# Performance work log

Hardware: AMD Instinct MI355X
Metric: run time of the kernel (lower is better)

Reference implementation:

```python
import jax, jax.numpy as jnp
import numpy as np

BS, S, D, H, L, DEG = 16, 512, 256, 4, 6, 16
N = BS * S
E = N * DEG
DH = D // H
LN_EPS = 1e-5


def _ln(x, w, b):
    mu = jnp.mean(x, -1, keepdims=True)
    var = jnp.var(x, -1, keepdims=True)
    return (x - mu) * jax.lax.rsqrt(var + LN_EPS) * w + b


def _gine(x, src, dst, ea, eps, ew, eb, w1, b1, w2, b2):
    # PyG GINEConv: nn((1+eps)*x_i + sum_j relu(x_j + lin(e_ji))), msgs flow src->dst
    msg = jax.nn.relu(x[src] + ea @ ew.T + eb)
    agg = jax.ops.segment_sum(msg, dst, num_segments=x.shape[0])
    z = (1.0 + eps) * x + agg
    return jax.nn.relu(z @ w1.T + b1) @ w2.T + b2


def setup_inputs():
    key = jax.random.key(0)
    ks = iter(jax.random.split(key, 64))
    def rnd(shape, scale=0.05):
        return jax.random.normal(next(ks), shape, jnp.float32) * scale
    rng = np.random.default_rng(0)
    sl = rng.integers(0, S, E)
    dl = rng.integers(0, S, E)
    gid = np.repeat(np.arange(BS), S * DEG)
    edge_index = jnp.asarray(np.stack([sl + gid * S, dl + gid * S]), jnp.int32)
    ptr = jnp.asarray(np.arange(BS + 1) * S, jnp.int32)
    drop_edge_label = jnp.asarray(rng.integers(0, 2, E), jnp.int32)
    return dict(
        x=rnd((N, 2), 1.0),
        edge_attr=jax.random.uniform(next(ks), (E, 1), jnp.float32),
        eps1=jnp.zeros(()), edge_w1=rnd((2, 1)), edge_b1=jnp.zeros((2,)),
        nn1_w1=rnd((64, 2)), nn1_b1=jnp.zeros((64,)),
        nn1_w2=rnd((128, 64)), nn1_b2=jnp.zeros((128,)),
        eps2=jnp.zeros(()), edge_w2=rnd((128, 1)), edge_b2=jnp.zeros((128,)),
        nn2_w1=rnd((D, 128)), nn2_b1=jnp.zeros((D,)),
        nn2_w2=rnd((D, D)), nn2_b2=jnp.zeros((D,)),
        pos_emb=rnd((512, D), 0.02),
        in_proj_w=rnd((L, 3 * D, D)), in_proj_b=jnp.zeros((L, 3 * D)),
        out_proj_w=rnd((L, D, D)), out_proj_b=jnp.zeros((L, D)),
        ln1_w=jnp.ones((L, D)), ln1_b=jnp.zeros((L, D)),
        ln2_w=jnp.ones((L, D)), ln2_b=jnp.zeros((L, D)),
        ff_w1=rnd((L, 2 * D, D)), ff_b1=jnp.zeros((L, 2 * D)),
        ff_w2=rnd((L, D, 2 * D)), ff_b2=jnp.zeros((L, D)),
        fn_w=jnp.ones((D,)), fn_b=jnp.zeros((D,)),
        edge_index=edge_index, ptr=ptr, drop_edge_label=drop_edge_label,
    )


def _forward(x, edge_attr, eps1, edge_w1, edge_b1, nn1_w1, nn1_b1, nn1_w2, nn1_b2,
             eps2, edge_w2, edge_b2, nn2_w1, nn2_b1, nn2_w2, nn2_b2, pos_emb,
             in_proj_w, in_proj_b, out_proj_w, out_proj_b, ln1_w, ln1_b, ln2_w, ln2_b,
             ff_w1, ff_b1, ff_w2, ff_b2, fn_w, fn_b, edge_index, drop_edge_label):
    src, dst = edge_index[0], edge_index[1]
    h = jax.nn.relu(_gine(x, src, dst, edge_attr, eps1, edge_w1, edge_b1,
                          nn1_w1, nn1_b1, nn1_w2, nn1_b2))
    h = _gine(h, src, dst, edge_attr, eps2, edge_w2, edge_b2,
              nn2_w1, nn2_b1, nn2_w2, nn2_b2)
    # equal-size graphs -> batchify is a reshape
    xb = h.reshape(BS, S, D) + pos_emb[:S]
    # graph-derived additive attention mask (src_mask of 1s with 0s at dropped edges,
    # symmetric), plus the float key_padding_mask (all ones here) -- both ADDED to
    # attention logits exactly as torch MultiheadAttention does with float masks.
    g = src // S
    ls = src - g * S
    ld = dst - g * S
    keep = (1 - drop_edge_label).astype(jnp.float32)
    adj = jnp.ones((BS, S, S), jnp.float32)
    adj = adj.at[g, ls, ld].min(keep).at[g, ld, ls].min(keep)
    bias = adj[:, None, :, :] + 1.0  # [BS,1,S,S], broadcast over heads
    scale = 1.0 / jnp.sqrt(jnp.float32(DH))
    for l in range(L):  # norm_first encoder layers, dropout disabled
        hn = _ln(xb, ln1_w[l], ln1_b[l])
        qkv = hn @ in_proj_w[l].T + in_proj_b[l]
        q, k, v = jnp.split(qkv, 3, axis=-1)
        q = q.reshape(BS, S, H, DH).transpose(0, 2, 1, 3)
        k = k.reshape(BS, S, H, DH).transpose(0, 2, 1, 3)
        v = v.reshape(BS, S, H, DH).transpose(0, 2, 1, 3)
        scores = jnp.einsum('bhqd,bhkd->bhqk', q, k) * scale + bias
        attn = jax.nn.softmax(scores, axis=-1)
        o = jnp.einsum('bhqk,bhkd->bhqd', attn, v).transpose(0, 2, 1, 3).reshape(BS, S, D)
        xb = xb + o @ out_proj_w[l].T + out_proj_b[l]
        hn = _ln(xb, ln2_w[l], ln2_b[l])
        xb = xb + jax.nn.silu(hn @ ff_w1[l].T + ff_b1[l]) @ ff_w2[l].T + ff_b2[l]
    return _ln(xb, fn_w, fn_b)


def reference(x, edge_attr, eps1, edge_w1, edge_b1, nn1_w1, nn1_b1, nn1_w2, nn1_b2,
              eps2, edge_w2, edge_b2, nn2_w1, nn2_b1, nn2_w2, nn2_b2, pos_emb,
              in_proj_w, in_proj_b, out_proj_w, out_proj_b, ln1_w, ln1_b, ln2_w, ln2_b,
              ff_w1, ff_b1, ff_w2, ff_b2, fn_w, fn_b, edge_index, ptr, drop_edge_label):
    return _forward(x, edge_attr, eps1, edge_w1, edge_b1, nn1_w1, nn1_b1, nn1_w2, nn1_b2,
                    eps2, edge_w2, edge_b2, nn2_w1, nn2_b1, nn2_w2, nn2_b2, pos_emb,
                    in_proj_w, in_proj_b, out_proj_w, out_proj_b, ln1_w, ln1_b, ln2_w, ln2_b,
                    ff_w1, ff_b1, ff_w2, ff_b2, fn_w, fn_b, edge_index, drop_edge_label)
```

## Files before the change

### kernel.cpp

```cpp
#include <hip/hip_runtime.h>

#define BSZ 16
#define SQ  512
#define DM  256
#define NHD 4
#define NLY 6
#define NND 8192
#define NEG 131072
#define DHD 64

typedef float  f32x4  __attribute__((ext_vector_type(4)));
typedef __bf16 bf16x8 __attribute__((ext_vector_type(8)));

#define N_SRC 31
struct SrcPtrs { const void* p[N_SRC]; };

__device__ __host__ __forceinline__ long asz_at(int i) {
    const int asz[N_SRC] = {16384, 131072, 1, 2, 2, 128, 64, 8192, 128, 1, 128, 128,
                            32768, 256, 65536, 256, 131072, 1179648, 4608, 393216, 1536,
                            1536, 1536, 1536, 1536, 786432, 3072, 786432, 1536, 256, 256};
    return asz[i];
}

__global__ void convert_arena(SrcPtrs sp, __bf16* __restrict__ arena, long total) {
    long gid = (long)blockIdx.x * 256 + threadIdx.x;
    if (gid >= total) return;
    bool isbf = (*(const unsigned int*)sp.p[21]) == 0x3F803F80u;
    long off = 0;
    #pragma unroll
    for (int i = 0; i < N_SRC; i++) {
        long sz = asz_at(i), pad = (sz + 15) & ~15L;
        if (gid >= off && gid < off + sz) {
            long k = gid - off;
            float v = isbf ? (float)((const __bf16*)sp.p[i])[k]
                           : ((const float*)sp.p[i])[k];
            arena[gid] = (__bf16)v;
        }
        off += pad;
    }
}

__global__ void gine1_edge(const __bf16* __restrict__ x, const __bf16* __restrict__ ea,
                           const int* __restrict__ src, const int* __restrict__ dst,
                           const __bf16* __restrict__ ew, const __bf16* __restrict__ eb,
                           float* __restrict__ agg) {
    int e = blockIdx.x * 256 + threadIdx.x;
    if (e >= NEG) return;
    float a = (float)ea[e];
    int s = src[e], d = dst[e];
    float m0 = (float)x[s * 2 + 0] + a * (float)ew[0] + (float)eb[0];
    float m1 = (float)x[s * 2 + 1] + a * (float)ew[1] + (float)eb[1];
    if (m0 > 0.f) atomicAdd(&agg[d * 2 + 0], m0);
    if (m1 > 0.f) atomicAdd(&agg[d * 2 + 1], m1);
}

__global__ void gine1_node(const __bf16* __restrict__ x, const float* __restrict__ agg,
                           const __bf16* __restrict__ eps,
                           const __bf16* __restrict__ w1, const __bf16* __restrict__ b1,
                           const __bf16* __restrict__ w2, const __bf16* __restrict__ b2,
                           float* __restrict__ h1f) {
    __shared__ float hid[2][64];
    int hl = threadIdx.x >> 7, c = threadIdx.x & 127;
    int n = blockIdx.x * 2 + hl;
    float e1 = 1.f + (float)eps[0];
    float z0 = e1 * (float)x[n * 2 + 0] + agg[n * 2 + 0];
    float z1 = e1 * (float)x[n * 2 + 1] + agg[n * 2 + 1];
    if (c < 64) {
        float h = z0 * (float)w1[c * 2 + 0] + z1 * (float)w1[c * 2 + 1] + (float)b1[c];
        hid[hl][c] = h > 0.f ? h : 0.f;
    }
    __syncthreads();
    float s = (float)b2[c];
    #pragma unroll
    for (int h = 0; h < 64; h++) s += hid[hl][h] * (float)w2[c * 64 + h];
    h1f[(long)n * 128 + c] = s > 0.f ? s : 0.f;
}

__global__ void gine2_edge(const float* __restrict__ h1f, const __bf16* __restrict__ ea,
                           const int* __restrict__ src, const int* __restrict__ dst,
                           const __bf16* __restrict__ ew, const __bf16* __restrict__ eb,
                           float* __restrict__ agg) {
    long gid = (long)blockIdx.x * 256 + threadIdx.x;
    int e = (int)(gid >> 7), c = (int)(gid & 127);
    float m = h1f[(long)src[e] * 128 + c] + (float)ea[e] * (float)ew[c] + (float)eb[c];
    if (m > 0.f) atomicAdd(&agg[(long)dst[e] * 128 + c], m);
}

__global__ void make_z2(const float* __restrict__ h1f, const float* __restrict__ agg,
                        const __bf16* __restrict__ eps, __bf16* __restrict__ z2b) {
    long gid = (long)blockIdx.x * 256 + threadIdx.x;
    float e1 = 1.f + (float)eps[0];
    z2b[gid] = (__bf16)(e1 * h1f[gid] + agg[gid]);
}

__global__ void drop_mask(const int* __restrict__ src, const int* __restrict__ dst,
                          const int* __restrict__ drop, unsigned int* __restrict__ mask) {
    int e = blockIdx.x * 256 + threadIdx.x;
    if (e >= NEG) return;
    if (drop[e]) {
        int s = src[e], d = dst[e];
        int b = s >> 9, ls = s & 511, ld = d & 511;
        atomicOr(&mask[((long)(b * 512 + ls)) * 16 + (ld >> 5)], 1u << (ld & 31));
        atomicOr(&mask[((long)(b * 512 + ld)) * 16 + (ls >> 5)], 1u << (ls & 31));
    }
}

__global__ __launch_bounds__(256) void ln_k(const float* __restrict__ xin,
                                            const __bf16* __restrict__ w,
                                            const __bf16* __restrict__ b,
                                            __bf16* __restrict__ out) {
    int lane = threadIdx.x & 63;
    int row = blockIdx.x * 4 + (threadIdx.x >> 6);
    const float* xr = xin + (long)row * 256;
    f32x4 v = *(const f32x4*)(xr + lane * 4);
    float s  = v[0] + v[1] + v[2] + v[3];
    float s2 = v[0]*v[0] + v[1]*v[1] + v[2]*v[2] + v[3]*v[3];
    #pragma unroll
    for (int o = 32; o > 0; o >>= 1) { s += __shfl_xor(s, o); s2 += __shfl_xor(s2, o); }
    float mean = s * (1.f / 256.f);
    float var  = s2 * (1.f / 256.f) - mean * mean;
    float rstd = rsqrtf(var + 1e-5f);
    __attribute__((aligned(8))) __bf16 o4[4];
    #pragma unroll
    for (int k = 0; k < 4; k++)
        o4[k] = (__bf16)((v[k] - mean) * rstd * (float)w[lane * 4 + k] + (float)b[lane * 4 + k]);
    *(unsigned long long*)(out + (long)row * 256 + lane * 4) = *(const unsigned long long*)o4;
}

__global__ __launch_bounds__(256) void ln_out(const float* __restrict__ xin,
                                              const __bf16* __restrict__ w,
                                              const __bf16* __restrict__ b,
                                              float* __restrict__ out) {
    int lane = threadIdx.x & 63;
    int row = blockIdx.x * 4 + (threadIdx.x >> 6);
    const float* xr = xin + (long)row * 256;
    f32x4 v = *(const f32x4*)(xr + lane * 4);
    float s  = v[0] + v[1] + v[2] + v[3];
    float s2 = v[0]*v[0] + v[1]*v[1] + v[2]*v[2] + v[3]*v[3];
    #pragma unroll
    for (int o = 32; o > 0; o >>= 1) { s += __shfl_xor(s, o); s2 += __shfl_xor(s2, o); }
    float mean = s * (1.f / 256.f);
    float var  = s2 * (1.f / 256.f) - mean * mean;
    float rstd = rsqrtf(var + 1e-5f);
    f32x4 o4;
    #pragma unroll
    for (int k = 0; k < 4; k++)
        o4[k] = (v[k] - mean) * rstd * (float)w[lane * 4 + k] + (float)b[lane * 4 + k];
    *(f32x4*)(out + (long)row * 256 + lane * 4) = o4;
}

__device__ __forceinline__ void gload_lds16(const void* g, void* l) {
    __builtin_amdgcn_global_load_lds(
        (const __attribute__((address_space(1))) void*)g,
        (__attribute__((address_space(3))) void*)l, 16, 0, 0);
}

__device__ __forceinline__ void stage_tile64(const __bf16* A, const __bf16* W,
                                             long tm, long tn, int K, int k0,
                                             __bf16* bA, __bf16* bB, int w, int lane) {
    int lin = w * 1024 + lane * 16;
    gload_lds16((const char*)A + ((tm + (lin >> 6)) * K + k0) * 2 + (lin & 63),
                (char*)bA + lin);
    gload_lds16((const char*)W + ((tn + (lin >> 6)) * K + k0) * 2 + (lin & 63),
                (char*)bB + lin);
}

__global__ __launch_bounds__(256) void gemm_bt(
        const __bf16* __restrict__ A, const __bf16* __restrict__ W,
        const __bf16* __restrict__ bias, __bf16* __restrict__ outb,
        float* __restrict__ outf, const float* __restrict__ resid,
        const __bf16* __restrict__ pos, __bf16* __restrict__ vT,
        int K, int ldout, int act, int qkvmode) {
    __shared__ __attribute__((aligned(16))) __bf16 lA[2][64 * 32];
    __shared__ __attribute__((aligned(16))) __bf16 lB[2][64 * 32];
    const int tid = threadIdx.x, lane = tid & 63, w = tid >> 6;
    const int wm = w & 1, wn = w >> 1;
    const int quad = lane >> 4, l16 = lane & 15;
    const long tm = (long)blockIdx.x * 64, tn = (long)blockIdx.y * 64;
    f32x4 acc[2][2] = {};
    stage_tile64(A, W, tm, tn, K, 0, lA[0], lB[0], w, lane);
    int buf = 0;
    for (int k0 = 0; k0 < K; k0 += 32, buf ^= 1) {
        __syncthreads();
        if (k0 + 32 < K)
            stage_tile64(A, W, tm, tn, K, k0 + 32, lA[buf ^ 1], lB[buf ^ 1], w, lane);
        const __bf16* bA = lA[buf];
        const __bf16* bB = lB[buf];
        const int kg = quad * 8;
        bf16x8 af[2], bfv[2];
        #pragma unroll
        for (int i = 0; i < 2; i++) af[i]  = *(const bf16x8*)&bA[(wm * 32 + i * 16 + l16) * 32 + kg];
        #pragma unroll
        for (int j = 0; j < 2; j++) bfv[j] = *(const bf16x8*)&bB[(wn * 32 + j * 16 + l16) * 32 + kg];
        #pragma unroll
        for (int i = 0; i < 2; i++)
            #pragma unroll
            for (int j = 0; j < 2; j++)
                acc[i][j] = __builtin_amdgcn_mfma_f32_16x16x32_bf16(af[i], bfv[j], acc[i][j], 0, 0, 0);
    }
    #pragma unroll
    for (int i = 0; i < 2; i++) {
        #pragma unroll
        for (int j = 0; j < 2; j++) {
            #pragma unroll
            for (int r = 0; r < 4; r++) {
                int m = (int)tm + wm * 32 + i * 16 + quad * 4 + r;
                int n = (int)tn + wn * 32 + j * 16 + l16;
                float v = acc[i][j][r];
                if (bias) v += (float)bias[n];
                if (act == 1) v = v > 0.f ? v : 0.f;
                else if (act == 2) v = v / (1.f + __expf(-v));
                if (qkvmode) {
                    if (n < 512) {
                        if (n < 256) v *= 0.125f;
                        outb[(long)m * ldout + n] = (__bf16)v;
                    } else {
                        int vc = n - 512, hh = vc >> 6, d = vc & 63;
                        int b = m >> 9, sdx = m & 511;
                        vT[(((long)(b * NHD + hh) * DHD + d) << 9) + sdx] = (__bf16)v;
                    }
                } else if (outf) {
                    if (resid) v += resid[(long)m * ldout + n];
                    if (pos)   v += (float)pos[(long)(m & 511) * ldout + n];
                    outf[(long)m * ldout + n] = v;
                } else {
                    outb[(long)m * ldout + n] = (__bf16)v;
                }
            }
        }
    }
}

__global__ __launch_bounds__(256) void attn_fused(const __bf16* __restrict__ qk,
                                                  const __bf16* __restrict__ vT,
                                                  const unsigned int* __restrict__ mask,
                                                  __bf16* __restrict__ attno) {
    __shared__ __bf16 pt[4][16 * 512];
    const int lane = threadIdx.x & 63, w = threadIdx.x >> 6;
    const int qb = blockIdx.x, h = blockIdx.y, b = blockIdx.z;
    const int qr0 = qb * 64 + w * 16;
    const int quad = lane >> 4, l16 = lane & 15;
    const int bh = b * NHD + h;
    const __bf16* qbase = qk + ((long)(b * 512 + qr0 + l16)) * 512 + h * 64 + quad * 8;
    bf16x8 qf0 = *(const bf16x8*)(qbase);
    bf16x8 qf1 = *(const bf16x8*)(qbase + 32);
    f32x4 acc[32];
    #pragma unroll
    for (int t = 0; t < 32; t++) {
        const __bf16* kbase = qk + ((long)(b * 512 + t * 16 + l16)) * 512 + 256 + h * 64 + quad * 8;
        bf16x8 kf0 = *(const bf16x8*)(kbase);
        bf16x8 kf1 = *(const bf16x8*)(kbase + 32);
        f32x4 z = {0.f, 0.f, 0.f, 0.f};
        z = __builtin_amdgcn_mfma_f32_16x16x32_bf16(qf0, kf0, z, 0, 0, 0);
        acc[t] = __builtin_amdgcn_mfma_f32_16x16x32_bf16(qf1, kf1, z, 0, 0, 0);
    }
    const unsigned int* mrow = mask + ((long)(b * 512 + qr0 + quad * 4)) * 16;
    float mx[4] = {-1e30f, -1e30f, -1e30f, -1e30f};
    #pragma unroll
    for (int t = 0; t < 32; t++)
        #pragma unroll
        for (int r = 0; r < 4; r++) {
            unsigned int wd = mrow[r * 16 + (t >> 1)];
            float bias = 2.f - (float)((wd >> (((t & 1) << 4) + l16)) & 1u);
            float v = acc[t][r] + bias;
            acc[t][r] = v;
            mx[r] = fmaxf(mx[r], v);
        }
    #pragma unroll
    for (int r = 0; r < 4; r++)
        #pragma unroll
        for (int o = 1; o < 16; o <<= 1) mx[r] = fmaxf(mx[r], __shfl_xor(mx[r], o));
    float sm[4] = {0.f, 0.f, 0.f, 0.f};
    #pragma unroll
    for (int t = 0; t < 32; t++)
        #pragma unroll
        for (int r = 0; r < 4; r++) {
            float e = __expf(acc[t][r] - mx[r]);
            acc[t][r] = e;
            sm[r] += e;
        }
    #pragma unroll
    for (int r = 0; r < 4; r++)
        #pragma unroll
        for (int o = 1; o < 16; o <<= 1) sm[r] += __shfl_xor(sm[r], o);
    float inv[4];
    #pragma unroll
    for (int r = 0; r < 4; r++) inv[r] = 1.f / sm[r];
    #pragma unroll
    for (int t = 0; t < 32; t++)
        #pragma unroll
        for (int r = 0; r < 4; r++)
            pt[w][(quad * 4 + r) * 512 + t * 16 + l16] = (__bf16)(acc[t][r] * inv[r]);
    __syncthreads();
    f32x4 oacc[4] = {};
    for (int kk = 0; kk < 512; kk += 32) {
        bf16x8 pf = *(const bf16x8*)&pt[w][l16 * 512 + kk + quad * 8];
        #pragma unroll
        for (int j = 0; j < 4; j++) {
            const __bf16* vrow = vT + ((long)bh * 64 + j * 16 + l16) * 512 + kk + quad * 8;
            bf16x8 vf = *(const bf16x8*)(vrow);
            oacc[j] = __builtin_amdgcn_mfma_f32_16x16x32_bf16(pf, vf, oacc[j], 0, 0, 0);
        }
    }
    #pragma unroll
    for (int j = 0; j < 4; j++)
        #pragma unroll
        for (int r = 0; r < 4; r++) {
            int m = qr0 + quad * 4 + r, d = j * 16 + l16;
            attno[((long)(b * 512 + m)) * 256 + h * 64 + d] = (__bf16)oacc[j][r];
        }
}

extern "C" void kernel_launch(void* const* d_in, const int* in_sizes, int n_in,
                              void* d_out, int out_size, void* d_ws, size_t ws_size,
                              hipStream_t stream) {
    const long MB = 1024 * 1024;

    const int* ei   = (const int*)d_in[31];
    const int* drop = (const int*)d_in[33];
    const int* esrc = ei;
    const int* edst = ei + NEG;

    char* ws = (char*)d_ws;
    float*  xb    = (float*)(ws + 0);
    __bf16* arena = (__bf16*)(ws + 8 * MB);
    unsigned int* maskw = (unsigned int*)(ws + 15 * MB + 512 * 1024);
    float*  agg1  = (float*)(ws + 16 * MB);
    float*  agg2  = (float*)(ws + 17 * MB);
    float*  h1f   = (float*)(ws + 21 * MB);
    __bf16* z2b   = (__bf16*)(ws + 25 * MB);
    __bf16* t1b   = (__bf16*)(ws + 27 * MB);
    __bf16* hnb   = (__bf16*)(ws + 31 * MB);
    __bf16* qkb   = (__bf16*)(ws + 35 * MB);
    __bf16* vT    = (__bf16*)(ws + 43 * MB);
    __bf16* attno = (__bf16*)(ws + 47 * MB);
    __bf16* ff1b  = (__bf16*)(ws + 51 * MB);

    SrcPtrs sp;
    __bf16* ap[N_SRC];
    long off = 0;
    for (int i = 0; i < N_SRC; i++) {
        sp.p[i] = d_in[i];
        ap[i] = arena + off;
        off += (asz_at(i) + 15) & ~15L;
    }
    convert_arena<<<(int)((off + 255) / 256), 256, 0, stream>>>(sp, arena, off);

    const __bf16 *xA = ap[0], *eaA = ap[1], *eps1A = ap[2], *ew1A = ap[3], *eb1A = ap[4],
                 *n1w1A = ap[5], *n1b1A = ap[6], *n1w2A = ap[7], *n1b2A = ap[8],
                 *eps2A = ap[9], *ew2A = ap[10], *eb2A = ap[11],
                 *n2w1A = ap[12], *n2b1A = ap[13], *n2w2A = ap[14], *n2b2A = ap[15],
                 *posA = ap[16], *ipwA = ap[17], *ipbA = ap[18], *opwA = ap[19], *opbA = ap[20],
                 *ln1wA = ap[21], *ln1bA = ap[22], *ln2wA = ap[23], *ln2bA = ap[24],
                 *f1wA = ap[25], *f1bA = ap[26], *f2wA = ap[27], *f2bA = ap[28],
                 *fnwA = ap[29], *fnbA = ap[30];

    hipMemsetAsync(agg1, 0, (size_t)NND * 2 * 4, stream);
    hipMemsetAsync(agg2, 0, (size_t)NND * 128 * 4, stream);
    hipMemsetAsync(maskw, 0, (size_t)512 * 1024, stream);

    gine1_edge<<<NEG / 256, 256, 0, stream>>>(xA, eaA, esrc, edst, ew1A, eb1A, agg1);
    gine1_node<<<NND / 2, 256, 0, stream>>>(xA, agg1, eps1A, n1w1A, n1b1A, n1w2A, n1b2A, h1f);
    gine2_edge<<<(NEG * 128) / 256, 256, 0, stream>>>(h1f, eaA, esrc, edst, ew2A, eb2A, agg2);
    make_z2<<<(NND * 128) / 256, 256, 0, stream>>>(h1f, agg2, eps2A, z2b);

    gemm_bt<<<dim3(NND / 64, 4), 256, 0, stream>>>(z2b, n2w1A, n2b1A, t1b, nullptr, nullptr, nullptr, nullptr,
                                                   128, 256, 1, 0);
    gemm_bt<<<dim3(NND / 64, 4), 256, 0, stream>>>(t1b, n2w2A, n2b2A, nullptr, xb, nullptr, posA, nullptr,
                                                   256, 256, 0, 0);

    drop_mask<<<NEG / 256, 256, 0, stream>>>(esrc, edst, drop, maskw);

    for (int l = 0; l < NLY; l++) {
        ln_k<<<NND / 4, 256, 0, stream>>>(xb, ln1wA + l * 256, ln1bA + l * 256, hnb);
        gemm_bt<<<dim3(NND / 64, 12), 256, 0, stream>>>(hnb, ipwA + (long)l * 768 * 256, ipbA + l * 768,
                                                        qkb, nullptr, nullptr, nullptr, vT,
                                                        256, 512, 0, 1);
        attn_fused<<<dim3(8, NHD, BSZ), 256, 0, stream>>>(qkb, vT, maskw, attno);
        gemm_bt<<<dim3(NND / 64, 4), 256, 0, stream>>>(attno, opwA + (long)l * 256 * 256, opbA + l * 256,
                                                       nullptr, xb, xb, nullptr, nullptr,
                                                       256, 256, 0, 0);
        ln_k<<<NND / 4, 256, 0, stream>>>(xb, ln2wA + l * 256, ln2bA + l * 256, hnb);
        gemm_bt<<<dim3(NND / 64, 8), 256, 0, stream>>>(hnb, f1wA + (long)l * 512 * 256, f1bA + l * 512,
                                                       ff1b, nullptr, nullptr, nullptr, nullptr,
                                                       256, 512, 2, 0);
        gemm_bt<<<dim3(NND / 64, 4), 256, 0, stream>>>(ff1b, f2wA + (long)l * 256 * 512, f2bA + l * 256,
                                                       nullptr, xb, xb, nullptr, nullptr,
                                                       512, 256, 0, 0);
    }
    ln_out<<<NND / 4, 256, 0, stream>>>(xb, fnwA, fnbA, (float*)d_out);
}
```

Measured before the change: 890.0 us.

## Replace GINE2 atomic scatter with CSR gather and deepen GEMM K-step

```diff
diff --git a/kernel.cpp b/kernel.cpp
--- a/kernel.cpp
+++ b/kernel.cpp
@@ -76,21 +76,52 @@
     h1f[(long)n * 128 + c] = s > 0.f ? s : 0.f;
 }
 
-__global__ void gine2_edge(const float* __restrict__ h1f, const __bf16* __restrict__ ea,
-                           const int* __restrict__ src, const int* __restrict__ dst,
-                           const __bf16* __restrict__ ew, const __bf16* __restrict__ eb,
-                           float* __restrict__ agg) {
-    long gid = (long)blockIdx.x * 256 + threadIdx.x;
-    int e = (int)(gid >> 7), c = (int)(gid & 127);
-    float m = h1f[(long)src[e] * 128 + c] + (float)ea[e] * (float)ew[c] + (float)eb[c];
-    if (m > 0.f) atomicAdd(&agg[(long)dst[e] * 128 + c], m);
-}
-
-__global__ void make_z2(const float* __restrict__ h1f, const float* __restrict__ agg,
-                        const __bf16* __restrict__ eps, __bf16* __restrict__ z2b) {
-    long gid = (long)blockIdx.x * 256 + threadIdx.x;
+__global__ void csr_hist(const int* __restrict__ dst, int* __restrict__ deg) {
+    int e = blockIdx.x * 256 + threadIdx.x;
+    if (e < NEG) atomicAdd(&deg[dst[e]], 1);
+}
+__global__ void csr_scan(const int* __restrict__ deg, int* __restrict__ ptr) {
+    __shared__ int part[256];
+    __shared__ int pref[256];
+    int t = threadIdx.x, base = t * 32;
+    int s = 0;
+    for (int i = 0; i < 32; i++) s += deg[base + i];
+    part[t] = s;
+    __syncthreads();
+    if (t == 0) { int run = 0; for (int i = 0; i < 256; i++) { pref[i] = run; run += part[i]; } }
+    __syncthreads();
+    int run = pref[t];
+    for (int i = 0; i < 32; i++) { ptr[base + i] = run; run += deg[base + i]; }
+    if (t == 255) ptr[NND] = run;
+}
+__global__ void csr_copy(const int* __restrict__ ptr, int* __restrict__ pos) {
+    int i = blockIdx.x * 256 + threadIdx.x;
+    if (i < NND) pos[i] = ptr[i];
+}
+__global__ void csr_scatter(const int* __restrict__ dst, int* __restrict__ pos,
+                            int* __restrict__ elist) {
+    int e = blockIdx.x * 256 + threadIdx.x;
+    if (e >= NEG) return;
+    elist[atomicAdd(&pos[dst[e]], 1)] = e;
+}
+__global__ __launch_bounds__(128) void gine2_gather(
+        const float* __restrict__ h1f, const __bf16* __restrict__ ea,
+        const int* __restrict__ src, const int* __restrict__ ptr,
+        const int* __restrict__ elist, const __bf16* __restrict__ eps,
+        const __bf16* __restrict__ ew, const __bf16* __restrict__ eb,
+        __bf16* __restrict__ z2b) {
+    int n = blockIdx.x, c = threadIdx.x;
+    int beg = ptr[n], end = ptr[n + 1];
+    float ewc = (float)ew[c], ebc = (float)eb[c];
+    float acc = 0.f;
+    for (int j = beg; j < end; j++) {
+        int e = elist[j];
+        float m = h1f[(long)src[e] * 128 + c] + (float)ea[e] * ewc + ebc;
+        acc += m > 0.f ? m : 0.f;
+    }
     float e1 = 1.f + (float)eps[0];
-    z2b[gid] = (__bf16)(e1 * h1f[gid] + agg[gid]);
+    long o = (long)n * 128 + c;
+    z2b[o] = (__bf16)(e1 * h1f[o] + acc);
 }
 
 __global__ void drop_mask(const int* __restrict__ src, const int* __restrict__ dst,
@@ -155,14 +186,11 @@
         (__attribute__((address_space(3))) void*)l, 16, 0, 0);
 }
 
-__device__ __forceinline__ void stage_tile64(const __bf16* A, const __bf16* W,
-                                             long tm, long tn, int K, int k0,
-                                             __bf16* bA, __bf16* bB, int w, int lane) {
+__device__ __forceinline__ void stage_panel(const __bf16* G, long trow, int K, int k0,
+                                            __bf16* panel, int w, int lane) {
     int lin = w * 1024 + lane * 16;
-    gload_lds16((const char*)A + ((tm + (lin >> 6)) * K + k0) * 2 + (lin & 63),
-                (char*)bA + lin);
-    gload_lds16((const char*)W + ((tn + (lin >> 6)) * K + k0) * 2 + (lin & 63),
-                (char*)bB + lin);
+    gload_lds16((const char*)G + ((trow + (lin >> 6)) * K + k0) * 2 + (lin & 63),
+                (char*)panel + lin);
 }
 
 __global__ __launch_bounds__(256) void gemm_bt(
@@ -171,32 +199,42 @@
         float* __restrict__ outf, const float* __restrict__ resid,
         const __bf16* __restrict__ pos, __bf16* __restrict__ vT,
         int K, int ldout, int act, int qkvmode) {
-    __shared__ __attribute__((aligned(16))) __bf16 lA[2][64 * 32];
-    __shared__ __attribute__((aligned(16))) __bf16 lB[2][64 * 32];
+    __shared__ __attribute__((aligned(16))) __bf16 lA[2][2][64 * 32];
+    __shared__ __attribute__((aligned(16))) __bf16 lB[2][2][64 * 32];
     const int tid = threadIdx.x, lane = tid & 63, w = tid >> 6;
     const int wm = w & 1, wn = w >> 1;
     const int quad = lane >> 4, l16 = lane & 15;
     const long tm = (long)blockIdx.x * 64, tn = (long)blockIdx.y * 64;
     f32x4 acc[2][2] = {};
-    stage_tile64(A, W, tm, tn, K, 0, lA[0], lB[0], w, lane);
+    stage_panel(A, tm, K, 0,  lA[0][0], w, lane);
+    stage_panel(A, tm, K, 32, lA[0][1], w, lane);
+    stage_panel(W, tn, K, 0,  lB[0][0], w, lane);
+    stage_panel(W, tn, K, 32, lB[0][1], w, lane);
     int buf = 0;
-    for (int k0 = 0; k0 < K; k0 += 32, buf ^= 1) {
+    for (int k0 = 0; k0 < K; k0 += 64, buf ^= 1) {
         __syncthreads();
-        if (k0 + 32 < K)
-            stage_tile64(A, W, tm, tn, K, k0 + 32, lA[buf ^ 1], lB[buf ^ 1], w, lane);
-        const __bf16* bA = lA[buf];
-        const __bf16* bB = lB[buf];
+        if (k0 + 64 < K) {
+            stage_panel(A, tm, K, k0 + 64, lA[buf ^ 1][0], w, lane);
+            stage_panel(A, tm, K, k0 + 96, lA[buf ^ 1][1], w, lane);
+            stage_panel(W, tn, K, k0 + 64, lB[buf ^ 1][0], w, lane);
+            stage_panel(W, tn, K, k0 + 96, lB[buf ^ 1][1], w, lane);
+        }
         const int kg = quad * 8;
-        bf16x8 af[2], bfv[2];
-        #pragma unroll
-        for (int i = 0; i < 2; i++) af[i]  = *(const bf16x8*)&bA[(wm * 32 + i * 16 + l16) * 32 + kg];
-        #pragma unroll
-        for (int j = 0; j < 2; j++) bfv[j] = *(const bf16x8*)&bB[(wn * 32 + j * 16 + l16) * 32 + kg];
-        #pragma unroll
-        for (int i = 0; i < 2; i++)
+        #pragma unroll
+        for (int half = 0; half < 2; half++) {
+            const __bf16* bA = lA[buf][half];
+            const __bf16* bB = lB[buf][half];
+            bf16x8 af[2], bfv[2];
             #pragma unroll
-            for (int j = 0; j < 2; j++)
-                acc[i][j] = __builtin_amdgcn_mfma_f32_16x16x32_bf16(af[i], bfv[j], acc[i][j], 0, 0, 0);
+            for (int i = 0; i < 2; i++) af[i]  = *(const bf16x8*)&bA[(wm * 32 + i * 16 + l16) * 32 + kg];
+            #pragma unroll
+            for (int j = 0; j < 2; j++) bfv[j] = *(const bf16x8*)&bB[(wn * 32 + j * 16 + l16) * 32 + kg];
+            #pragma unroll
+            for (int i = 0; i < 2; i++)
+                #pragma unroll
+                for (int j = 0; j < 2; j++)
+                    acc[i][j] = __builtin_amdgcn_mfma_f32_16x16x32_bf16(af[i], bfv[j], acc[i][j], 0, 0, 0);
+        }
     }
     #pragma unroll
     for (int i = 0; i < 2; i++) {
@@ -326,7 +364,10 @@
     __bf16* arena = (__bf16*)(ws + 8 * MB);
     unsigned int* maskw = (unsigned int*)(ws + 15 * MB + 512 * 1024);
     float*  agg1  = (float*)(ws + 16 * MB);
-    float*  agg2  = (float*)(ws + 17 * MB);
+    int*    deg   = (int*)(ws + 17 * MB);
+    int*    ptrc  = (int*)(ws + 17 * MB + 64 * 1024);
+    int*    posc  = (int*)(ws + 17 * MB + 128 * 1024);
+    int*    elist = (int*)(ws + 17 * MB + 192 * 1024);
     float*  h1f   = (float*)(ws + 21 * MB);
     __bf16* z2b   = (__bf16*)(ws + 25 * MB);
     __bf16* t1b   = (__bf16*)(ws + 27 * MB);
@@ -356,13 +397,17 @@
                  *fnwA = ap[29], *fnbA = ap[30];
 
     hipMemsetAsync(agg1, 0, (size_t)NND * 2 * 4, stream);
-    hipMemsetAsync(agg2, 0, (size_t)NND * 128 * 4, stream);
+    hipMemsetAsync(deg, 0, (size_t)NND * 4, stream);
     hipMemsetAsync(maskw, 0, (size_t)512 * 1024, stream);
+
+    csr_hist<<<NEG / 256, 256, 0, stream>>>(edst, deg);
+    csr_scan<<<1, 256, 0, stream>>>(deg, ptrc);
+    csr_copy<<<NND / 256, 256, 0, stream>>>(ptrc, posc);
+    csr_scatter<<<NEG / 256, 256, 0, stream>>>(edst, posc, elist);
 
     gine1_edge<<<NEG / 256, 256, 0, stream>>>(xA, eaA, esrc, edst, ew1A, eb1A, agg1);
     gine1_node<<<NND / 2, 256, 0, stream>>>(xA, agg1, eps1A, n1w1A, n1b1A, n1w2A, n1b2A, h1f);
-    gine2_edge<<<(NEG * 128) / 256, 256, 0, stream>>>(h1f, eaA, esrc, edst, ew2A, eb2A, agg2);
-    make_z2<<<(NND * 128) / 256, 256, 0, stream>>>(h1f, agg2, eps2A, z2b);
+    gine2_gather<<<NND, 128, 0, stream>>>(h1f, eaA, esrc, ptrc, elist, eps2A, ew2A, eb2A, z2b);
 
     gemm_bt<<<dim3(NND / 64, 4), 256, 0, stream>>>(z2b, n2w1A, n2b1A, t1b, nullptr, nullptr, nullptr, nullptr,
                                                    128, 256, 1, 0);
```

After: 886.1 us. Within noise of the previous version (-0.4%).
